# Kernel optimization log

Hardware: AMD Instinct MI355X
Metric: run time of the kernel (lower is better)

The kernel has to match this reference:

```python
import jax, jax.numpy as jnp
import numpy as np

N = 8192
D = 256
LN_EPS = 1e-5
NORM_EPS = 1e-12


def _layernorm(h, gamma, beta):
    mu = jnp.mean(h, axis=-1, keepdims=True)
    var = jnp.var(h, axis=-1, keepdims=True)
    return (h - mu) * jax.lax.rsqrt(var + LN_EPS) * gamma + beta


def _elu(z):
    return jnp.where(z > 0, z, jnp.expm1(z))


def setup_inputs() -> dict:
    key = jax.random.key(0)
    ks = jax.random.split(key, 5)
    s = 1.0 / np.sqrt(D)  # torch Linear default-ish init scale
    h = jax.random.normal(ks[0], (N, D), dtype=jnp.float32)
    x = jax.random.normal(ks[1], (N, D), dtype=jnp.float32)
    Wk = jax.random.normal(ks[2], (D, D), dtype=jnp.float32) * s
    Wq = jax.random.normal(ks[3], (D, D), dtype=jnp.float32) * s
    Wv = jax.random.normal(ks[4], (D, D), dtype=jnp.float32) * s
    ln_gamma = jnp.ones((D,), dtype=jnp.float32)
    ln_beta = jnp.zeros((D,), dtype=jnp.float32)
    semantic_weight = -1.0
    mixing = jnp.array([[semantic_weight, semantic_weight], [0.0, 0.0]], dtype=jnp.float32)
    return {"h": h, "x": x, "Wk": Wk, "Wq": Wq, "Wv": Wv,
            "ln_gamma": ln_gamma, "ln_beta": ln_beta, "mixing": mixing}


def reference(h, x, Wk, Wq, Wv, ln_gamma, ln_beta, mixing):
    h0, x0 = h, x
    hn = _layernorm(h, ln_gamma, ln_beta)                      # [N, D]
    k = hn @ Wk                                                # [N, H]
    q = hn @ Wq                                                # [N, H]
    # semantic attention: softmax over rows of k q^T / sqrt(H)
    a_h = jax.nn.softmax((k @ q.T) * (D ** -0.5), axis=-1)     # [N, N]
    # structural attention: row-L2-normalized gram matrix of x
    g = x @ x.T                                                # [N, N]
    gnorm = jnp.linalg.norm(g, axis=-1, keepdims=True)
    a_x = g / jnp.maximum(gnorm, NORM_EPS)
    # learned 2x2 mixing, softmax over dim 0 (stack @ mixing.softmax(0))
    m = jax.nn.softmax(mixing, axis=0)
    a_h_mix = a_h * m[0, 0] + a_x * m[1, 0]
    a_x_mix = a_h * m[0, 1] + a_x * m[1, 1]
    h_new = _elu((a_h_mix @ hn) @ Wv)                          # [N, D]
    x_new = a_x_mix @ x                                        # [N, D]
    h_new = h_new + h0
    x_new = x_new + x0
    return (h_new, x_new)
```

## Files before the change

kernel.cpp:

```cpp
#include <hip/hip_runtime.h>

#define N 8192
#define D 256

typedef unsigned short u16;
typedef unsigned int u32;
typedef short bf16x8 __attribute__((ext_vector_type(8)));
typedef float f32x4 __attribute__((ext_vector_type(4)));

__device__ __forceinline__ u16 f2bf(float f) {
    u32 u = __float_as_uint(f);
    u += 0x7FFFu + ((u >> 16) & 1u);
    return (u16)(u >> 16);
}
__device__ __forceinline__ float bf2f(u16 v) {
    return __uint_as_float(((u32)v) << 16);
}

#define MFMA(a, b, c) __builtin_amdgcn_mfma_f32_16x16x32_bf16((a), (b), (c), 0, 0, 0)

__global__ __launch_bounds__(256) void k_prep_ln(const float* __restrict__ h,
    const float* __restrict__ x, const float* __restrict__ gamma,
    const float* __restrict__ beta, u16* __restrict__ hnb, u16* __restrict__ xb)
{
    int lane = threadIdx.x & 63;
    int row = blockIdx.x * 4 + (threadIdx.x >> 6);
    const float4 hv = ((const float4*)(h + (size_t)row * D))[lane];
    float s = hv.x + hv.y + hv.z + hv.w;
    float s2 = hv.x * hv.x + hv.y * hv.y + hv.z * hv.z + hv.w * hv.w;
#pragma unroll
    for (int m = 1; m < 64; m <<= 1) { s += __shfl_xor(s, m); s2 += __shfl_xor(s2, m); }
    float mu = s * (1.0f / D);
    float var = s2 * (1.0f / D) - mu * mu;
    float rstd = rsqrtf(var + 1e-5f);
    const float4 gv = ((const float4*)gamma)[lane];
    const float4 bv = ((const float4*)beta)[lane];
    ushort4 o;
    o.x = f2bf((hv.x - mu) * rstd * gv.x + bv.x);
    o.y = f2bf((hv.y - mu) * rstd * gv.y + bv.y);
    o.z = f2bf((hv.z - mu) * rstd * gv.z + bv.z);
    o.w = f2bf((hv.w - mu) * rstd * gv.w + bv.w);
    ((ushort4*)(hnb + (size_t)row * D))[lane] = o;
    const float4 xv = ((const float4*)(x + (size_t)row * D))[lane];
    ushort4 xo;
    xo.x = f2bf(xv.x); xo.y = f2bf(xv.y); xo.z = f2bf(xv.z); xo.w = f2bf(xv.w);
    ((ushort4*)(xb + (size_t)row * D))[lane] = xo;
}

__global__ void k_wT(const float* __restrict__ Wk, const float* __restrict__ Wq,
                     const float* __restrict__ Wv, u16* __restrict__ wkT,
                     u16* __restrict__ wqT, u16* __restrict__ wvT)
{
    const float* src = blockIdx.y == 0 ? Wk : (blockIdx.y == 1 ? Wq : Wv);
    u16* dst = blockIdx.y == 0 ? wkT : (blockIdx.y == 1 ? wqT : wvT);
    int c = blockIdx.x, r = threadIdx.x;
    dst[c * D + r] = f2bf(src[r * D + c]);
}

__global__ __launch_bounds__(256) void k_transpose(const u16* __restrict__ s0,
    u16* __restrict__ d0, const u16* __restrict__ s1, u16* __restrict__ d1)
{
    const u16* src = blockIdx.y ? s1 : s0;
    u16* dst = blockIdx.y ? d1 : d0;
    int jb = (blockIdx.x & 127) * 64;
    int cb = (blockIdx.x >> 7) * 64;
    __shared__ u16 tile[64][72];
    int t = threadIdx.x;
#pragma unroll
    for (int i = 0; i < 2; ++i) {
        int id = t + i * 256;
        int r = id >> 3, ch = id & 7;
        uint4 v = *(const uint4*)(src + (size_t)(jb + r) * D + cb + ch * 8);
        *(uint4*)(&tile[r][ch * 8]) = v;
    }
    __syncthreads();
#pragma unroll
    for (int i = 0; i < 2; ++i) {
        int id = t + i * 256;
        int c = id >> 3, rch = id & 7;
        u16 vals[8] __attribute__((aligned(16)));
#pragma unroll
        for (int e = 0; e < 8; ++e) vals[e] = tile[rch * 8 + e][c];
        *(uint4*)(dst + (size_t)(cb + c) * N + jb + rch * 8) = *(const uint4*)vals;
    }
}

__global__ __launch_bounds__(256, 4) void k_proj_kq(const u16* __restrict__ A,
    const u16* __restrict__ wkT, const u16* __restrict__ wqT,
    u16* __restrict__ kb, u16* __restrict__ qb)
{
    int w = threadIdx.x >> 6;
    int lane = threadIdx.x & 63;
    int l16 = lane & 15, lhi = lane >> 4;
    int rows = blockIdx.x * 16;
    const u16* BT = (w >> 1) ? wqT : wkT;
    u16* out = (w >> 1) ? qb : kb;
    int colbase = (w & 1) * 128;
    const f32x4 z4 = {0.f, 0.f, 0.f, 0.f};
    f32x4 acc[8] = {z4, z4, z4, z4, z4, z4, z4, z4};
#pragma unroll
    for (int ks = 0; ks < 8; ++ks) {
        bf16x8 a = *(const bf16x8*)(A + (size_t)(rows + l16) * D + ks * 32 + lhi * 8);
#pragma unroll
        for (int cf = 0; cf < 8; ++cf) {
            bf16x8 b = *(const bf16x8*)(BT + (size_t)(colbase + cf * 16 + l16) * D + ks * 32 + lhi * 8);
            acc[cf] = MFMA(a, b, acc[cf]);
        }
    }
#pragma unroll
    for (int cf = 0; cf < 8; ++cf)
#pragma unroll
        for (int jj = 0; jj < 4; ++jj)
            out[(size_t)(rows + lhi * 4 + jj) * D + colbase + cf * 16 + l16] = f2bf(acc[cf][jj]);
}

__global__ __launch_bounds__(256) void k_small_nt(const u16* __restrict__ hnT,
    const u16* __restrict__ xT, float* __restrict__ part)
{
    const u16* P = blockIdx.y ? hnT : xT;
    const u16* Q = xT;
    int w = threadIdx.x >> 6;
    int lane = threadIdx.x & 63;
    int l16 = lane & 15, lhi = lane >> 4;
    int arow = blockIdx.x * 16;
    int bcol = w * 64;
    int n0b = blockIdx.z * 1024;
    const f32x4 z4 = {0.f, 0.f, 0.f, 0.f};
    f32x4 acc[4] = {z4, z4, z4, z4};
    for (int n0 = n0b; n0 < n0b + 1024; n0 += 32) {
        bf16x8 a = *(const bf16x8*)(P + (size_t)(arow + l16) * N + n0 + lhi * 8);
#pragma unroll
        for (int cf = 0; cf < 4; ++cf) {
            bf16x8 b = *(const bf16x8*)(Q + (size_t)(bcol + cf * 16 + l16) * N + n0 + lhi * 8);
            acc[cf] = MFMA(a, b, acc[cf]);
        }
    }
    float* dst = part + ((size_t)blockIdx.z * 2 + blockIdx.y) * 65536;
#pragma unroll
    for (int cf = 0; cf < 4; ++cf)
#pragma unroll
        for (int jj = 0; jj < 4; ++jj)
            dst[(size_t)(arow + lhi * 4 + jj) * D + bcol + cf * 16 + l16] = acc[cf][jj];
}

__global__ __launch_bounds__(256) void k_cast(const float* __restrict__ part,
    u16* __restrict__ Mb, u16* __restrict__ XHT)
{
    int t = blockIdx.x * 256 + threadIdx.x;
    int side = t >> 16, idx = t & 65535;
    float s = 0.f;
#pragma unroll
    for (int ks = 0; ks < 8; ++ks) s += part[((size_t)ks * 2 + side) * 65536 + idx];
    (side ? XHT : Mb)[idx] = f2bf(s);
}

template <int EPI>
__global__ __launch_bounds__(256, 4) void k_gemm16(const u16* __restrict__ A,
    const u16* __restrict__ BT, u16* __restrict__ outb,
    const float* __restrict__ res, float* __restrict__ outf)
{
    int w = threadIdx.x >> 6;
    int lane = threadIdx.x & 63;
    int l16 = lane & 15, lhi = lane >> 4;
    int rows = blockIdx.x * 16;
    int cols = w * 64;
    const f32x4 z4 = {0.f, 0.f, 0.f, 0.f};
    f32x4 acc[4] = {z4, z4, z4, z4};
#pragma unroll
    for (int ks = 0; ks < 8; ++ks) {
        bf16x8 a = *(const bf16x8*)(A + (size_t)(rows + l16) * D + ks * 32 + lhi * 8);
#pragma unroll
        for (int cf = 0; cf < 4; ++cf) {
            bf16x8 b = *(const bf16x8*)(BT + (size_t)(cols + cf * 16 + l16) * D + ks * 32 + lhi * 8);
            acc[cf] = MFMA(a, b, acc[cf]);
        }
    }
#pragma unroll
    for (int cf = 0; cf < 4; ++cf)
#pragma unroll
        for (int jj = 0; jj < 4; ++jj) {
            int r = rows + lhi * 4 + jj;
            int c = cols + cf * 16 + l16;
            float v = acc[cf][jj];
            if (EPI == 0) {
                outb[(size_t)r * D + c] = f2bf(v);
            } else {
                float z = v > 0.f ? v : expm1f(v);
                outf[(size_t)r * D + c] = z + res[(size_t)r * D + c];
            }
        }
}

__global__ __launch_bounds__(512, 4) void k_fused(const u16* __restrict__ kb,
    const u16* __restrict__ qb, const u16* __restrict__ hnT,
    const u16* __restrict__ xT, u16* __restrict__ accP, float* __restrict__ lpart)
{
    __shared__ u16 AK[64 * 256];
    __shared__ u16 P[64 * 256];
    const int tid = threadIdx.x;
    const int w = tid >> 6;
    const int lane = tid & 63;
    const int l16 = lane & 15, lhi = lane >> 4;
    const int wgid = blockIdx.x;
    const int xcd = wgid & 7;
    const int js = xcd >> 1;
    const int rb = ((wgid >> 3) << 1) | (xcd & 1);
    const int R0 = rb * 64;
    const int jbase = js * 2048;

    {
        int r = tid >> 3, sb = (tid & 7) * 4;
        const u16* src = kb + (size_t)(R0 + r) * D + sb * 8;
#pragma unroll
        for (int i = 0; i < 4; ++i) {
            bf16x8 v = *(const bf16x8*)(src + i * 8);
            int s = sb + i;
            int slotp = (s & 16) | ((s & 15) ^ (r & 15));
            *(bf16x8*)(AK + r * 256 + slotp * 8) = v;
        }
    }
    __syncthreads();

    const int rg = w & 1;
    const int jf = w >> 1;
    const int t2 = w >> 2;
    const int ch = w & 3;
    const u16* T = t2 ? xT : hnT;
    const u16* Tb0 = T + (size_t)(ch * 64 + 0 * 16 + l16) * N + lhi * 8;
    const u16* Tb1 = T + (size_t)(ch * 64 + 1 * 16 + l16) * N + lhi * 8;
    const u16* Tb2 = T + (size_t)(ch * 64 + 2 * 16 + l16) * N + lhi * 8;
    const u16* Tb3 = T + (size_t)(ch * 64 + 3 * 16 + l16) * N + lhi * 8;

    const f32x4 z4 = {0.f, 0.f, 0.f, 0.f};
    f32x4 acc[16];
#pragma unroll
    for (int i = 0; i < 16; ++i) acc[i] = z4;
    f32x4 red2[2] = {z4, z4};
    bf16x8 tp0[4], tp1[4];

    for (int it = 0; it < 8; ++it) {
        const int jb = jbase + it * 256;
        asm volatile("s_waitcnt lgkmcnt(0)\n\ts_barrier" ::: "memory");

#pragma unroll
        for (int s = 0; s < 2; ++s) {
            const int jc = jb + s * 128 + jf * 32;
            f32x4 cs00 = z4, cs01 = z4, cs10 = z4, cs11 = z4;
#pragma unroll
            for (int ks = 0; ks < 8; ++ks) {
                int r0 = rg * 32 + l16;
                int r1 = rg * 32 + 16 + l16;
                int sq = ks * 4 + lhi;
                int slx = (sq & 16) | ((sq & 15) ^ l16);
                bf16x8 a0 = *(const bf16x8*)(AK + r0 * 256 + slx * 8);
                bf16x8 a1 = *(const bf16x8*)(AK + r1 * 256 + slx * 8);
                const u16* Bq = qb + (size_t)(jc + l16) * D + ks * 32 + lhi * 8;
                bf16x8 b0 = *(const bf16x8*)(Bq);
                bf16x8 b1 = *(const bf16x8*)(Bq + 16 * D);
                cs00 = MFMA(a0, b0, cs00);
                cs01 = MFMA(a0, b1, cs01);
                cs10 = MFMA(a1, b0, cs10);
                cs11 = MFMA(a1, b1, cs11);
            }
#pragma unroll
            for (int rf = 0; rf < 2; ++rf)
#pragma unroll
                for (int cfr = 0; cfr < 2; ++cfr) {
                    f32x4 s4 = rf ? (cfr ? cs11 : cs10) : (cfr ? cs01 : cs00);
#pragma unroll
                    for (int jj = 0; jj < 4; ++jj) {
                        int row = rg * 32 + rf * 16 + lhi * 4 + jj;
                        int col = s * 128 + jf * 32 + cfr * 16 + l16;
                        float pv = __expf(s4[jj] * 0.0625f);
                        red2[rf][jj] += pv;
                        int slot = (col >> 3) ^ (row & 15);
                        *(u16*)((char*)P + row * 512 + slot * 16 + (col & 7) * 2) = f2bf(pv);
                    }
                }
        }
        tp0[0] = *(const bf16x8*)(Tb0 + jb); tp0[1] = *(const bf16x8*)(Tb1 + jb);
        tp0[2] = *(const bf16x8*)(Tb2 + jb); tp0[3] = *(const bf16x8*)(Tb3 + jb);
        tp1[0] = *(const bf16x8*)(Tb0 + jb + 32); tp1[1] = *(const bf16x8*)(Tb1 + jb + 32);
        tp1[2] = *(const bf16x8*)(Tb2 + jb + 32); tp1[3] = *(const bf16x8*)(Tb3 + jb + 32);
        asm volatile("s_waitcnt lgkmcnt(0)\n\ts_barrier" ::: "memory");

        __builtin_amdgcn_s_setprio(1);
        const char* Pb = (const char*)P;
#define PV_STEP(KF, TP)                                                             \
        {                                                                           \
            bf16x8 pa0 = *(const bf16x8*)(Pb + (0 * 16 + l16) * 512 + ((((KF) * 4 + lhi) ^ l16) << 4)); \
            bf16x8 pa1 = *(const bf16x8*)(Pb + (1 * 16 + l16) * 512 + ((((KF) * 4 + lhi) ^ l16) << 4)); \
            bf16x8 pa2 = *(const bf16x8*)(Pb + (2 * 16 + l16) * 512 + ((((KF) * 4 + lhi) ^ l16) << 4)); \
            bf16x8 pa3 = *(const bf16x8*)(Pb + (3 * 16 + l16) * 512 + ((((KF) * 4 + lhi) ^ l16) << 4)); \
            acc[0]  = MFMA(pa0, TP[0], acc[0]);  acc[1]  = MFMA(pa0, TP[1], acc[1]);  \
            acc[2]  = MFMA(pa0, TP[2], acc[2]);  acc[3]  = MFMA(pa0, TP[3], acc[3]);  \
            acc[4]  = MFMA(pa1, TP[0], acc[4]);  acc[5]  = MFMA(pa1, TP[1], acc[5]);  \
            acc[6]  = MFMA(pa1, TP[2], acc[6]);  acc[7]  = MFMA(pa1, TP[3], acc[7]);  \
            acc[8]  = MFMA(pa2, TP[0], acc[8]);  acc[9]  = MFMA(pa2, TP[1], acc[9]);  \
            acc[10] = MFMA(pa2, TP[2], acc[10]); acc[11] = MFMA(pa2, TP[3], acc[11]); \
            acc[12] = MFMA(pa3, TP[0], acc[12]); acc[13] = MFMA(pa3, TP[1], acc[13]); \
            acc[14] = MFMA(pa3, TP[2], acc[14]); acc[15] = MFMA(pa3, TP[3], acc[15]); \
            if ((KF) + 2 < 8) {                                                     \
                TP[0] = *(const bf16x8*)(Tb0 + jb + ((KF) + 2) * 32);               \
                TP[1] = *(const bf16x8*)(Tb1 + jb + ((KF) + 2) * 32);               \
                TP[2] = *(const bf16x8*)(Tb2 + jb + ((KF) + 2) * 32);               \
                TP[3] = *(const bf16x8*)(Tb3 + jb + ((KF) + 2) * 32);               \
            }                                                                       \
        }
        PV_STEP(0, tp0)
        PV_STEP(1, tp1)
        PV_STEP(2, tp0)
        PV_STEP(3, tp1)
        PV_STEP(4, tp0)
        PV_STEP(5, tp1)
        PV_STEP(6, tp0)
        PV_STEP(7, tp1)
#undef PV_STEP
        __builtin_amdgcn_s_setprio(0);
    }

    {
        u16* base = accP + ((((size_t)js * 128 + rb) * 8 + w) * 64) * 64 + lane;
#pragma unroll
        for (int rf = 0; rf < 4; ++rf)
#pragma unroll
            for (int cf = 0; cf < 4; ++cf)
#pragma unroll
                for (int jj = 0; jj < 4; ++jj) {
                    int v = (rf * 4 + cf) * 4 + jj;
                    __builtin_nontemporal_store(f2bf(acc[rf * 4 + cf][jj]), base + (size_t)v * 64);
                }
    }
#pragma unroll
    for (int rf = 0; rf < 2; ++rf)
#pragma unroll
        for (int m = 1; m < 16; m <<= 1) {
            red2[rf][0] += __shfl_xor(red2[rf][0], m);
            red2[rf][1] += __shfl_xor(red2[rf][1], m);
            red2[rf][2] += __shfl_xor(red2[rf][2], m);
            red2[rf][3] += __shfl_xor(red2[rf][3], m);
        }
    if (l16 == 0)
#pragma unroll
        for (int rf = 0; rf < 2; ++rf)
#pragma unroll
            for (int jj = 0; jj < 4; ++jj)
                atomicAdd(lpart + R0 + rg * 32 + rf * 16 + lhi * 4 + jj, red2[rf][jj]);
}

__global__ __launch_bounds__(256) void k_stats(const float* __restrict__ lpart,
    const u16* __restrict__ Ux, const u16* __restrict__ xb,
    const float* __restrict__ mixing, float* __restrict__ stats)
{
    int lane = threadIdx.x & 63;
    int row = blockIdx.x * 4 + (threadIdx.x >> 6);
    float sg = 0.f;
    {
        ushort4 yv = ((const ushort4*)(Ux + (size_t)row * D))[lane];
        ushort4 xv = ((const ushort4*)(xb + (size_t)row * D))[lane];
        sg += bf2f(yv.x) * bf2f(xv.x);
        sg += bf2f(yv.y) * bf2f(xv.y);
        sg += bf2f(yv.z) * bf2f(xv.z);
        sg += bf2f(yv.w) * bf2f(xv.w);
    }
#pragma unroll
    for (int m = 1; m < 64; m <<= 1) sg += __shfl_xor(sg, m);
    if (lane == 0) {
        float inv_l = 1.0f / lpart[row];
        float inv_g = 1.0f / fmaxf(sqrtf(fmaxf(sg, 0.f)), 1e-12f);
        float e00 = __expf(mixing[0]), e10 = __expf(mixing[2]);
        float c00 = e00 / (e00 + e10), c10 = e10 / (e00 + e10);
        float e01 = __expf(mixing[1]), e11 = __expf(mixing[3]);
        float c01 = e01 / (e01 + e11), c11 = e11 / (e01 + e11);
        float4 stv = { c00 * inv_l, c10 * inv_g, c01 * inv_l, c11 * inv_g };
        ((float4*)stats)[row] = stv;
    }
}

__global__ __launch_bounds__(256) void k_combine(const u16* __restrict__ accP,
    const float* __restrict__ stats, const u16* __restrict__ Uh,
    const u16* __restrict__ Ux, const float* __restrict__ x0,
    u16* __restrict__ hmixb, float* __restrict__ outx)
{
    int t = blockIdx.x * 256 + threadIdx.x;
    int r = t >> 7;
    int q = t & 127;
    int rb = r >> 6, rr = r & 63;
    int t2 = q >> 6;
    int cc = (q & 63) * 4;
    int wv = t2 * 4 + (cc >> 6);
    int rf = rr >> 4, lhi = (rr >> 2) & 3, jj = rr & 3;
    int cf = (cc >> 4) & 3, l16 = cc & 15;
    int v = (rf * 4 + cf) * 4 + jj;
    int lane = lhi * 16 + l16;
    float v0 = 0.f, v1 = 0.f, v2 = 0.f, v3 = 0.f;
#pragma unroll
    for (int s = 0; s < 4; ++s) {
        const u16* bp = accP + ((((size_t)s * 128 + rb) * 8 + wv) * 64 + v) * 64 + lane;
        ushort4 a = *(const ushort4*)bp;
        v0 += bf2f(a.x); v1 += bf2f(a.y); v2 += bf2f(a.z); v3 += bf2f(a.w);
    }
    float4 st = ((const float4*)stats)[r];
    if (t2 == 0) {
        int c = cc;
        ushort4 u = *(const ushort4*)(Uh + (size_t)r * D + c);
        ushort4 o;
        o.x = f2bf(st.x * v0 + st.y * bf2f(u.x));
        o.y = f2bf(st.x * v1 + st.y * bf2f(u.y));
        o.z = f2bf(st.x * v2 + st.y * bf2f(u.z));
        o.w = f2bf(st.x * v3 + st.y * bf2f(u.w));
        *(ushort4*)(hmixb + (size_t)r * D + c) = o;
    } else {
        int c = cc;
        ushort4 u = *(const ushort4*)(Ux + (size_t)r * D + c);
        float4 xv = *(const float4*)(x0 + (size_t)r * D + c);
        float4 o;
        o.x = st.z * v0 + st.w * bf2f(u.x) + xv.x;
        o.y = st.z * v1 + st.w * bf2f(u.y) + xv.y;
        o.z = st.z * v2 + st.w * bf2f(u.z) + xv.z;
        o.w = st.z * v3 + st.w * bf2f(u.w) + xv.w;
        *(float4*)(outx + (size_t)r * D + c) = o;
    }
}

extern "C" void kernel_launch(void* const* d_in, const int* in_sizes, int n_in,
                              void* d_out, int out_size, void* d_ws, size_t ws_size,
                              hipStream_t stream)
{
    const float* h = (const float*)d_in[0];
    const float* x = (const float*)d_in[1];
    const float* Wk = (const float*)d_in[2];
    const float* Wq = (const float*)d_in[3];
    const float* Wv = (const float*)d_in[4];
    const float* gamma = (const float*)d_in[5];
    const float* beta = (const float*)d_in[6];
    const float* mixing = (const float*)d_in[7];

    char* p = (char*)d_ws;
    const size_t ND2 = (size_t)N * D * 2;
    u16* hnb = (u16*)p; p += ND2;
    u16* xb = (u16*)p; p += ND2;
    u16* kb = (u16*)p; p += ND2;
    u16* qb = (u16*)p; p += ND2;
    u16* hnT = (u16*)p; p += ND2;
    u16* xT = (u16*)p; p += ND2;
    u16* Ux = (u16*)p; p += ND2;
    u16* wkT = (u16*)p; p += (size_t)D * D * 2;
    u16* wqT = (u16*)p; p += (size_t)D * D * 2;
    u16* wvT = (u16*)p; p += (size_t)D * D * 2;
    u16* Mb = (u16*)p; p += (size_t)D * D * 2;
    u16* XHT = (u16*)p; p += (size_t)D * D * 2;
    u16* accP = (u16*)p; p += (size_t)4 * N * 512 * 2;
    float* ntpart = (float*)accP;
    float* lpart = (float*)p; p += (size_t)N * 4;
    float* stats = (float*)p; p += (size_t)N * 4 * 4;
    u16* Uh = hnb;
    u16* hmixb = kb;

    float* outh = (float*)d_out;
    float* outx = outh + (size_t)N * D;

    hipMemsetAsync(lpart, 0, (size_t)N * 4, stream);
    k_prep_ln<<<N / 4, 256, 0, stream>>>(h, x, gamma, beta, hnb, xb);
    k_wT<<<dim3(256, 3), 256, 0, stream>>>(Wk, Wq, Wv, wkT, wqT, wvT);
    k_transpose<<<dim3(512, 2), 256, 0, stream>>>(hnb, hnT, xb, xT);
    k_proj_kq<<<512, 256, 0, stream>>>(hnb, wkT, wqT, kb, qb);
    k_small_nt<<<dim3(16, 2, 8), 256, 0, stream>>>(hnT, xT, ntpart);
    k_cast<<<512, 256, 0, stream>>>(ntpart, Mb, XHT);
    k_gemm16<0><<<512, 256, 0, stream>>>(xb, Mb, Ux, nullptr, nullptr);
    k_gemm16<0><<<512, 256, 0, stream>>>(xb, XHT, Uh, nullptr, nullptr);
    k_fused<<<512, 512, 0, stream>>>(kb, qb, hnT, xT, accP, lpart);
    k_stats<<<N / 4, 256, 0, stream>>>(lpart, Ux, xb, mixing, stats);
    k_combine<<<(N * 512) / 1024, 256, 0, stream>>>(accP, stats, Uh, Ux, x, hmixb, outx);
    k_gemm16<1><<<512, 256, 0, stream>>>(hmixb, wvT, nullptr, h, outh);
}
```

Baseline: 386.3 us.

## Double-buffer P tile and software-pipeline QK^T with PV across 128-column steps

```diff
diff --git a/kernel.cpp b/kernel.cpp
--- a/kernel.cpp
+++ b/kernel.cpp
@@ -196,7 +196,7 @@
     const u16* __restrict__ xT, u16* __restrict__ accP, float* __restrict__ lpart)
 {
     __shared__ u16 AK[64 * 256];
-    __shared__ u16 P[64 * 256];
+    __shared__ u16 P[2][64 * 136];
     const int tid = threadIdx.x;
     const int w = tid >> 6;
     const int lane = tid & 63;
@@ -219,7 +219,6 @@
             *(bf16x8*)(AK + r * 256 + slotp * 8) = v;
         }
     }
-    __syncthreads();
 
     const int rg = w & 1;
     const int jf = w >> 1;
@@ -238,60 +237,64 @@
     f32x4 red2[2] = {z4, z4};
     bf16x8 tp0[4], tp1[4];
 
-    for (int it = 0; it < 8; ++it) {
-        const int jb = jbase + it * 256;
+    auto S_body = [&](int it) {
+        const int jc = jbase + it * 128 + jf * 32;
+        u16* PW = &P[it & 1][0];
+        f32x4 cs00 = z4, cs01 = z4, cs10 = z4, cs11 = z4;
+#pragma unroll
+        for (int ks = 0; ks < 8; ++ks) {
+            int r0 = rg * 32 + l16;
+            int r1 = r0 + 16;
+            int sq = ks * 4 + lhi;
+            int slx = (sq & 16) | ((sq & 15) ^ l16);
+            bf16x8 a0 = *(const bf16x8*)(AK + r0 * 256 + slx * 8);
+            bf16x8 a1 = *(const bf16x8*)(AK + r1 * 256 + slx * 8);
+            const u16* Bq = qb + (size_t)(jc + l16) * D + ks * 32 + lhi * 8;
+            bf16x8 b0 = *(const bf16x8*)(Bq);
+            bf16x8 b1 = *(const bf16x8*)(Bq + 16 * D);
+            cs00 = MFMA(a0, b0, cs00);
+            cs01 = MFMA(a0, b1, cs01);
+            cs10 = MFMA(a1, b0, cs10);
+            cs11 = MFMA(a1, b1, cs11);
+        }
+#pragma unroll
+        for (int rf = 0; rf < 2; ++rf)
+#pragma unroll
+            for (int cfr = 0; cfr < 2; ++cfr) {
+                f32x4 s4 = rf ? (cfr ? cs11 : cs10) : (cfr ? cs01 : cs00);
+#pragma unroll
+                for (int jj = 0; jj < 4; ++jj) {
+                    int row = rg * 32 + rf * 16 + lhi * 4 + jj;
+                    int col = jf * 32 + cfr * 16 + l16;
+                    float pv = __expf(s4[jj] * 0.0625f);
+                    red2[rf][jj] += pv;
+                    int slot = (col >> 3) ^ (row & 15);
+                    *(u16*)((char*)PW + row * 272 + slot * 16 + (col & 7) * 2) = f2bf(pv);
+                }
+            }
+    };
+
+    __syncthreads();
+    S_body(0);
+
+    for (int it = 1; it <= 16; ++it) {
         asm volatile("s_waitcnt lgkmcnt(0)\n\ts_barrier" ::: "memory");
-
-#pragma unroll
-        for (int s = 0; s < 2; ++s) {
-            const int jc = jb + s * 128 + jf * 32;
-            f32x4 cs00 = z4, cs01 = z4, cs10 = z4, cs11 = z4;
-#pragma unroll
-            for (int ks = 0; ks < 8; ++ks) {
-                int r0 = rg * 32 + l16;
-                int r1 = rg * 32 + 16 + l16;
-                int sq = ks * 4 + lhi;
-                int slx = (sq & 16) | ((sq & 15) ^ l16);
-                bf16x8 a0 = *(const bf16x8*)(AK + r0 * 256 + slx * 8);
-                bf16x8 a1 = *(const bf16x8*)(AK + r1 * 256 + slx * 8);
-                const u16* Bq = qb + (size_t)(jc + l16) * D + ks * 32 + lhi * 8;
-                bf16x8 b0 = *(const bf16x8*)(Bq);
-                bf16x8 b1 = *(const bf16x8*)(Bq + 16 * D);
-                cs00 = MFMA(a0, b0, cs00);
-                cs01 = MFMA(a0, b1, cs01);
-                cs10 = MFMA(a1, b0, cs10);
-                cs11 = MFMA(a1, b1, cs11);
-            }
-#pragma unroll
-            for (int rf = 0; rf < 2; ++rf)
-#pragma unroll
-                for (int cfr = 0; cfr < 2; ++cfr) {
-                    f32x4 s4 = rf ? (cfr ? cs11 : cs10) : (cfr ? cs01 : cs00);
-#pragma unroll
-                    for (int jj = 0; jj < 4; ++jj) {
-                        int row = rg * 32 + rf * 16 + lhi * 4 + jj;
-                        int col = s * 128 + jf * 32 + cfr * 16 + l16;
-                        float pv = __expf(s4[jj] * 0.0625f);
-                        red2[rf][jj] += pv;
-                        int slot = (col >> 3) ^ (row & 15);
-                        *(u16*)((char*)P + row * 512 + slot * 16 + (col & 7) * 2) = f2bf(pv);
-                    }
-                }
-        }
-        tp0[0] = *(const bf16x8*)(Tb0 + jb); tp0[1] = *(const bf16x8*)(Tb1 + jb);
-        tp0[2] = *(const bf16x8*)(Tb2 + jb); tp0[3] = *(const bf16x8*)(Tb3 + jb);
-        tp1[0] = *(const bf16x8*)(Tb0 + jb + 32); tp1[1] = *(const bf16x8*)(Tb1 + jb + 32);
-        tp1[2] = *(const bf16x8*)(Tb2 + jb + 32); tp1[3] = *(const bf16x8*)(Tb3 + jb + 32);
-        asm volatile("s_waitcnt lgkmcnt(0)\n\ts_barrier" ::: "memory");
+        if (it < 16) S_body(it);
+
+        const int jbp = jbase + (it - 1) * 128;
+        const char* Pb = (const char*)&P[(it - 1) & 1][0];
+        tp0[0] = *(const bf16x8*)(Tb0 + jbp); tp0[1] = *(const bf16x8*)(Tb1 + jbp);
+        tp0[2] = *(const bf16x8*)(Tb2 + jbp); tp0[3] = *(const bf16x8*)(Tb3 + jbp);
+        tp1[0] = *(const bf16x8*)(Tb0 + jbp + 32); tp1[1] = *(const bf16x8*)(Tb1 + jbp + 32);
+        tp1[2] = *(const bf16x8*)(Tb2 + jbp + 32); tp1[3] = *(const bf16x8*)(Tb3 + jbp + 32);
 
         __builtin_amdgcn_s_setprio(1);
-        const char* Pb = (const char*)P;
 #define PV_STEP(KF, TP)                                                             \
         {                                                                           \
-            bf16x8 pa0 = *(const bf16x8*)(Pb + (0 * 16 + l16) * 512 + ((((KF) * 4 + lhi) ^ l16) << 4)); \
-            bf16x8 pa1 = *(const bf16x8*)(Pb + (1 * 16 + l16) * 512 + ((((KF) * 4 + lhi) ^ l16) << 4)); \
-            bf16x8 pa2 = *(const bf16x8*)(Pb + (2 * 16 + l16) * 512 + ((((KF) * 4 + lhi) ^ l16) << 4)); \
-            bf16x8 pa3 = *(const bf16x8*)(Pb + (3 * 16 + l16) * 512 + ((((KF) * 4 + lhi) ^ l16) << 4)); \
+            bf16x8 pa0 = *(const bf16x8*)(Pb + (0 * 16 + l16) * 272 + ((((KF) * 4 + lhi) ^ l16) << 4)); \
+            bf16x8 pa1 = *(const bf16x8*)(Pb + (1 * 16 + l16) * 272 + ((((KF) * 4 + lhi) ^ l16) << 4)); \
+            bf16x8 pa2 = *(const bf16x8*)(Pb + (2 * 16 + l16) * 272 + ((((KF) * 4 + lhi) ^ l16) << 4)); \
+            bf16x8 pa3 = *(const bf16x8*)(Pb + (3 * 16 + l16) * 272 + ((((KF) * 4 + lhi) ^ l16) << 4)); \
             acc[0]  = MFMA(pa0, TP[0], acc[0]);  acc[1]  = MFMA(pa0, TP[1], acc[1]);  \
             acc[2]  = MFMA(pa0, TP[2], acc[2]);  acc[3]  = MFMA(pa0, TP[3], acc[3]);  \
             acc[4]  = MFMA(pa1, TP[0], acc[4]);  acc[5]  = MFMA(pa1, TP[1], acc[5]);  \
@@ -300,21 +303,17 @@
             acc[10] = MFMA(pa2, TP[2], acc[10]); acc[11] = MFMA(pa2, TP[3], acc[11]); \
             acc[12] = MFMA(pa3, TP[0], acc[12]); acc[13] = MFMA(pa3, TP[1], acc[13]); \
             acc[14] = MFMA(pa3, TP[2], acc[14]); acc[15] = MFMA(pa3, TP[3], acc[15]); \
-            if ((KF) + 2 < 8) {                                                     \
-                TP[0] = *(const bf16x8*)(Tb0 + jb + ((KF) + 2) * 32);               \
-                TP[1] = *(const bf16x8*)(Tb1 + jb + ((KF) + 2) * 32);               \
-                TP[2] = *(const bf16x8*)(Tb2 + jb + ((KF) + 2) * 32);               \
-                TP[3] = *(const bf16x8*)(Tb3 + jb + ((KF) + 2) * 32);               \
+            if ((KF) + 2 < 4) {                                                     \
+                TP[0] = *(const bf16x8*)(Tb0 + jbp + ((KF) + 2) * 32);              \
+                TP[1] = *(const bf16x8*)(Tb1 + jbp + ((KF) + 2) * 32);              \
+                TP[2] = *(const bf16x8*)(Tb2 + jbp + ((KF) + 2) * 32);              \
+                TP[3] = *(const bf16x8*)(Tb3 + jbp + ((KF) + 2) * 32);              \
             }                                                                       \
         }
         PV_STEP(0, tp0)
         PV_STEP(1, tp1)
         PV_STEP(2, tp0)
         PV_STEP(3, tp1)
-        PV_STEP(4, tp0)
-        PV_STEP(5, tp1)
-        PV_STEP(6, tp0)
-        PV_STEP(7, tp1)
 #undef PV_STEP
         __builtin_amdgcn_s_setprio(0);
     }
```

New measurement: 395.6 us. 1.02x slower.
